# Kernel tuning notes

Hardware: AMD Instinct MI355X
Metric: run time of the kernel (lower is better)

## Reference

```python
import jax, jax.numpy as jnp
import numpy as np

B, S, D, H = 2, 2048, 1024, 16
HD = D // H

def setup_inputs() -> dict:
    key = jax.random.key(0)
    ks = jax.random.split(key, 5)
    s = 1.0 / np.sqrt(D)
    return {
        "x": jax.random.normal(ks[0], (B, S, D), dtype=jnp.float32),
        "Wq": jax.random.normal(ks[1], (D, D), dtype=jnp.float32) * s,
        "Wk": jax.random.normal(ks[2], (D, D), dtype=jnp.float32) * s,
        "Wv": jax.random.normal(ks[3], (D, D), dtype=jnp.float32) * s,
        "Wo": jax.random.normal(ks[4], (D, D), dtype=jnp.float32) * s,
        "bo": jnp.zeros((D,), dtype=jnp.float32),
    }

def reference(x, Wq, Wk, Wv, Wo, bo):
    b, n, _ = x.shape
    # QKV projections (no bias), reshape to [B, H, S, HD]
    def proj(W):
        return (x @ W.T).reshape(b, n, H, HD).transpose(0, 2, 1, 3)
    q, k, v = proj(Wq), proj(Wk), proj(Wv)
    scores = jnp.einsum("bhqd,bhkd->bhqk", q, k)
    causal = jnp.triu(jnp.ones((n, n), dtype=bool), k=1)
    scores = jnp.where(causal, -jnp.inf, scores)
    attn = jax.nn.softmax(scores / np.sqrt(HD), axis=-1)  # dropout p=0.0 (eval)
    ctx = jnp.einsum("bhqk,bhkd->bhqd", attn, v)
    ctx = ctx.transpose(0, 2, 1, 3).reshape(b, n, D)
    return ctx @ Wo.T + bo
```

## Files before the change

### kernel.cpp

```cpp
#include <hip/hip_runtime.h>
#include <stdint.h>


typedef __bf16 bf16_t;
typedef __bf16 bf16x8 __attribute__((ext_vector_type(8)));
typedef float  f32x4  __attribute__((ext_vector_type(4)));
typedef uint32_t u32x4 __attribute__((ext_vector_type(4)));

#define MFMA16(A, B, C) __builtin_amdgcn_mfma_f32_16x16x32_bf16(A, B, C, 0, 0, 0)

__device__ __forceinline__ void async_ld16(const bf16_t* g, bf16_t* l) {
  __builtin_amdgcn_global_load_lds(
      (const __attribute__((address_space(1))) void*)g,
      (__attribute__((address_space(3))) void*)l, 16, 0, 0);
}

__device__ __forceinline__ void cvt4(const float* s, bf16_t* d, int i4) {
  const float4 v = *(const float4*)(s + i4);
  union { uint64_t u; bf16_t h[4]; } pk;
  pk.h[0] = (bf16_t)v.x; pk.h[1] = (bf16_t)v.y;
  pk.h[2] = (bf16_t)v.z; pk.h[3] = (bf16_t)v.w;
  *(uint64_t*)(d + i4) = pk.u;
}

__global__ __launch_bounds__(256) void cvt_all(
    const float* __restrict__ sx, const float* __restrict__ s1,
    const float* __restrict__ s2, const float* __restrict__ s3,
    bf16_t* __restrict__ dx, bf16_t* __restrict__ d1,
    bf16_t* __restrict__ d2, bf16_t* __restrict__ d3) {
  const int y = blockIdx.y;
  if (y != 0 && blockIdx.x >= 1024) return;
  const int i4 = (blockIdx.x * 256 + threadIdx.x) * 4;
  const float* s = (y == 0) ? sx : (y == 1) ? s1 : (y == 2) ? s2 : s3;
  bf16_t*      d = (y == 0) ? dx : (y == 1) ? d1 : (y == 2) ? d2 : d3;
  cvt4(s, d, i4);
}

__global__ __launch_bounds__(256) void cvt_one(const float* __restrict__ s,
                                               bf16_t* __restrict__ d) {
  cvt4(s, d, (blockIdx.x * 256 + threadIdx.x) * 4);
}

__device__ __forceinline__ void gemm_core_async(const bf16_t* __restrict__ A,
                                                const bf16_t* __restrict__ W,
                                                bf16_t* __restrict__ D,
                                                float* __restrict__ Dout,
                                                const float* __restrict__ bias,
                                                int mode) {
  __shared__ __align__(16) bf16_t As[128 * 64];
  __shared__ __align__(16) bf16_t Bs[128 * 64];

  const int tid  = threadIdx.x;
  const int lane = tid & 63;
  const int w    = tid >> 6;
  const int quad = lane >> 4;
  const int l15  = lane & 15;
  const int bm   = blockIdx.y * 128;
  const int bn   = blockIdx.x * 128;
  const int wm   = (w >> 1) * 64;
  const int wn   = (w & 1) * 64;
  const int sr   = lane >> 3;
  const int sc   = lane & 7;

  f32x4 acc[4][4] = {};

  for (int k0 = 0; k0 < 1024; k0 += 64) {
#pragma unroll
    for (int j = 0; j < 4; ++j) {
      const int r0 = w * 32 + j * 8;
      const int r  = r0 + sr;
      const int c  = sc ^ (r & 7);
      async_ld16(A + (size_t)(bm + r) * 1024 + k0 + c * 8, &As[r0 * 64]);
      async_ld16(W + (size_t)(bn + r) * 1024 + k0 + c * 8, &Bs[r0 * 64]);
    }
    __syncthreads();
#pragma unroll
    for (int kk = 0; kk < 64; kk += 32) {
      const int ck = (kk >> 3) + quad;
      bf16x8 aF[4], bF[4];
#pragma unroll
      for (int mt = 0; mt < 4; ++mt) {
        const int r = wm + mt * 16 + l15;
        aF[mt] = *(const bf16x8*)&As[r * 64 + (ck ^ (r & 7)) * 8];
      }
#pragma unroll
      for (int nt = 0; nt < 4; ++nt) {
        const int r = wn + nt * 16 + l15;
        bF[nt] = *(const bf16x8*)&Bs[r * 64 + (ck ^ (r & 7)) * 8];
      }
#pragma unroll
      for (int mt = 0; mt < 4; ++mt)
#pragma unroll
        for (int nt = 0; nt < 4; ++nt)
          acc[mt][nt] = MFMA16(aF[mt], bF[nt], acc[mt][nt]);
    }
    __syncthreads();
  }

#pragma unroll
  for (int mt = 0; mt < 4; ++mt) {
#pragma unroll
    for (int nt = 0; nt < 4; ++nt) {
      const int n  = bn + wn + nt * 16 + l15;
      const int mb = bm + wm + mt * 16 + quad * 4;
      if (mode == 0) {
        const int h = n >> 6, hd = n & 63;
#pragma unroll
        for (int r = 0; r < 4; ++r) {
          const int m = mb + r;
          const int b = m >> 11, s = m & 2047;
          D[(size_t)b * 2097152 + (size_t)h * 131072 + (size_t)s * 64 + hd] =
              (bf16_t)acc[mt][nt][r];
        }
      } else if (mode == 1) {
        const int h = n >> 6, hd = n & 63;
        const int b = mb >> 11, s0 = mb & 2047;
        union { uint64_t u; bf16_t h4[4]; } pk;
#pragma unroll
        for (int r = 0; r < 4; ++r) pk.h4[r] = (bf16_t)acc[mt][nt][r];
        *(uint64_t*)(D + (size_t)b * 2097152 + (size_t)h * 131072 +
                     (size_t)hd * 2048 + s0) = pk.u;
      } else {
        const float bv = bias[n];
#pragma unroll
        for (int r = 0; r < 4; ++r) {
          const int m = mb + r;
          Dout[(size_t)m * 1024 + n] = acc[mt][nt][r] + bv;
        }
      }
    }
  }
}

__global__ __launch_bounds__(256, 2) void gemm_qkv_a(
    const bf16_t* __restrict__ X,  const bf16_t* __restrict__ Wq,
    const bf16_t* __restrict__ Wk, const bf16_t* __restrict__ Wv,
    bf16_t* __restrict__ Q, bf16_t* __restrict__ K, bf16_t* __restrict__ V) {
  const int z = blockIdx.z;
  const bf16_t* W = (z == 0) ? Wq : (z == 1) ? Wk : Wv;
  bf16_t*       D = (z == 0) ? Q  : (z == 1) ? K  : V;
  gemm_core_async(X, W, D, nullptr, nullptr, (z == 2) ? 1 : 0);
}

__global__ __launch_bounds__(256, 2) void gemm_out_a(
    const bf16_t* __restrict__ ctx, const bf16_t* __restrict__ Wo,
    float* __restrict__ out, const float* __restrict__ bo) {
  gemm_core_async(ctx, Wo, nullptr, out, bo, 2);
}

__global__ __launch_bounds__(256, 2) void attn(
    const bf16_t* __restrict__ Qw, const bf16_t* __restrict__ Kw,
    const bf16_t* __restrict__ Vw, bf16_t* __restrict__ ctx) {
  constexpr int LDK = 72, LDV = 136, LDP = 136;
  __shared__ __align__(16) bf16_t Ks[128 * LDK];
  __shared__ __align__(16) bf16_t Vts[64 * LDV];
  __shared__ __align__(16) bf16_t Ps[128 * LDP];

  const int tid  = threadIdx.x;
  const int lane = tid & 63;
  const int w    = tid >> 6;
  const int quad = lane >> 4;
  const int l15  = lane & 15;
  const int b    = blockIdx.z;
  const int h    = blockIdx.y;
  const size_t bh = (size_t)(b * 16 + h) * (size_t)(2048 * 64);
  const bf16_t* Qh = Qw + bh;
  const bf16_t* Kh = Kw + bh;
  const bf16_t* Vh = Vw + bh;

  const int srow = tid >> 3, schk = tid & 7;
  const int vrow = tid >> 4, vchk = tid & 15;

  const float sc_log2 = 0.125f * 1.44269504088896340736f;

  for (int pass = 0; pass < 2; ++pass) {
    const int qt = (pass == 0) ? blockIdx.x : 15 - blockIdx.x;

    __syncthreads();
    bf16_t* Qs = Ps;
    {
      u32x4 rq[4];
#pragma unroll
      for (int s2 = 0; s2 < 4; ++s2)
        rq[s2] = *(const u32x4*)(Qh + (size_t)(qt * 128 + srow + s2 * 32) * 64 + schk * 8);
#pragma unroll
      for (int s2 = 0; s2 < 4; ++s2)
        *(u32x4*)&Qs[(srow + s2 * 32) * LDK + schk * 8] = rq[s2];
    }
    __syncthreads();
    bf16x8 qF[2][2];
#pragma unroll
    for (int kq = 0; kq < 2; ++kq)
#pragma unroll
      for (int k2 = 0; k2 < 2; ++k2)
        qF[kq][k2] = *(const bf16x8*)
            &Qs[(w * 32 + kq * 16 + l15) * LDK + k2 * 32 + quad * 8];

    f32x4 O[2][4] = {};
    float mrow[2] = {-1e30f, -1e30f};
    float lrow[2] = {0.f, 0.f};

    u32x4 rk[4], rv[4];
#pragma unroll
    for (int s2 = 0; s2 < 4; ++s2)
      rk[s2] = *(const u32x4*)(Kh + (size_t)(srow + s2 * 32) * 64 + schk * 8);
#pragma unroll
    for (int s2 = 0; s2 < 4; ++s2)
      rv[s2] = *(const u32x4*)(Vh + (size_t)(vrow + s2 * 16) * 2048 + vchk * 8);

    for (int kt = 0; kt <= qt; ++kt) {
      __syncthreads();
#pragma unroll
      for (int s2 = 0; s2 < 4; ++s2)
        *(u32x4*)&Ks[(srow + s2 * 32) * LDK + schk * 8] = rk[s2];
#pragma unroll
      for (int s2 = 0; s2 < 4; ++s2)
        *(u32x4*)&Vts[(vrow + s2 * 16) * LDV + vchk * 8] = rv[s2];
      __syncthreads();

      if (kt < qt) {
        const int kn = kt + 1;
#pragma unroll
        for (int s2 = 0; s2 < 4; ++s2)
          rk[s2] = *(const u32x4*)(Kh + (size_t)(kn * 128 + srow + s2 * 32) * 64 + schk * 8);
#pragma unroll
        for (int s2 = 0; s2 < 4; ++s2)
          rv[s2] = *(const u32x4*)(Vh + (size_t)(vrow + s2 * 16) * 2048 + kn * 128 + vchk * 8);
      }

      f32x4 St[2][8] = {};
#pragma unroll
      for (int ntk = 0; ntk < 8; ++ntk) {
        const int kr = ntk * 16 + l15;
#pragma unroll
        for (int k2 = 0; k2 < 2; ++k2) {
          const bf16x8 kF = *(const bf16x8*)&Ks[kr * LDK + k2 * 32 + quad * 8];
#pragma unroll
          for (int kq = 0; kq < 2; ++kq)
            St[kq][ntk] = MFMA16(kF, qF[kq][k2], St[kq][ntk]);
        }
      }

      if (kt == qt) {
#pragma unroll
        for (int kq = 0; kq < 2; ++kq) {
          const int ql = w * 32 + kq * 16 + l15;
#pragma unroll
          for (int ntk = 0; ntk < 8; ++ntk)
#pragma unroll
            for (int r = 0; r < 4; ++r)
              if (ntk * 16 + quad * 4 + r > ql) St[kq][ntk][r] = -1e30f;
        }
      }

      float aq[2];
#pragma unroll
      for (int kq = 0; kq < 2; ++kq) {
        float mx = -1e30f;
#pragma unroll
        for (int ntk = 0; ntk < 8; ++ntk)
#pragma unroll
          for (int r = 0; r < 4; ++r) mx = fmaxf(mx, St[kq][ntk][r]);
        mx = fmaxf(mx, __shfl_xor(mx, 16));
        mx = fmaxf(mx, __shfl_xor(mx, 32));
        const float mnew  = fmaxf(mrow[kq], mx);
        const float alpha = exp2f((mrow[kq] - mnew) * sc_log2);
        mrow[kq] = mnew;
        float rs = 0.f;
#pragma unroll
        for (int ntk = 0; ntk < 8; ++ntk) {
          union { uint64_t u; bf16_t h4[4]; } pk;
#pragma unroll
          for (int r = 0; r < 4; ++r) {
            const float p = exp2f((St[kq][ntk][r] - mnew) * sc_log2);
            rs += p;
            pk.h4[r] = (bf16_t)p;
          }
          *(uint64_t*)&Ps[(w * 32 + kq * 16 + l15) * LDP + ntk * 16 + quad * 4] = pk.u;
        }
        rs += __shfl_xor(rs, 16);
        rs += __shfl_xor(rs, 32);
        lrow[kq] = lrow[kq] * alpha + rs;
        aq[kq] = alpha;
      }

#pragma unroll
      for (int mt = 0; mt < 2; ++mt) {
#pragma unroll
        for (int r = 0; r < 4; ++r) {
          const float a = __shfl(aq[mt], quad * 4 + r);
#pragma unroll
          for (int nt = 0; nt < 4; ++nt) O[mt][nt][r] *= a;
        }
      }

#pragma unroll
      for (int kk = 0; kk < 128; kk += 32) {
        const int co = kk + quad * 8;
        bf16x8 pF[2], vF[4];
#pragma unroll
        for (int mt = 0; mt < 2; ++mt)
          pF[mt] = *(const bf16x8*)&Ps[(w * 32 + mt * 16 + l15) * LDP + co];
#pragma unroll
        for (int nt = 0; nt < 4; ++nt)
          vF[nt] = *(const bf16x8*)&Vts[(nt * 16 + l15) * LDV + co];
#pragma unroll
        for (int mt = 0; mt < 2; ++mt)
#pragma unroll
          for (int nt = 0; nt < 4; ++nt)
            O[mt][nt] = MFMA16(pF[mt], vF[nt], O[mt][nt]);
      }
    }

#pragma unroll
    for (int mt = 0; mt < 2; ++mt) {
#pragma unroll
      for (int r = 0; r < 4; ++r) {
        const float lr = __shfl(lrow[mt], quad * 4 + r);
        const float iv = 1.f / lr;
        const int s = qt * 128 + w * 32 + mt * 16 + quad * 4 + r;
#pragma unroll
        for (int nt = 0; nt < 4; ++nt) {
          const int hd = nt * 16 + l15;
          ctx[(size_t)(b * 2048 + s) * 1024 + h * 64 + hd] =
              (bf16_t)(O[mt][nt][r] * iv);
        }
      }
    }
  }
}

extern "C" void kernel_launch(void* const* d_in, const int* in_sizes, int n_in,
                              void* d_out, int out_size, void* d_ws, size_t ws_size,
                              hipStream_t stream) {
  const float* x  = (const float*)d_in[0];
  const float* Wq = (const float*)d_in[1];
  const float* Wk = (const float*)d_in[2];
  const float* Wv = (const float*)d_in[3];
  const float* Wo = (const float*)d_in[4];
  const float* bo = (const float*)d_in[5];

  bf16_t* ws   = (bf16_t*)d_ws;
  bf16_t* Qw   = ws;
  bf16_t* Kw   = ws + 4194304;
  bf16_t* Vw   = ws + 8388608;
  bf16_t* ctxw = ws + 12582912;
  bf16_t* Wob  = Qw;

  bf16_t* dscr = (bf16_t*)d_out;
  bf16_t* xb   = dscr;
  bf16_t* Wqb  = dscr + 4194304;
  bf16_t* Wkb  = dscr + 5242880;
  bf16_t* Wvb  = dscr + 6291456;
  float*  out  = (float*)d_out;

  dim3 blk(256);
  cvt_all<<<dim3(4096, 4), blk, 0, stream>>>(x, Wq, Wk, Wv, xb, Wqb, Wkb, Wvb);
  gemm_qkv_a<<<dim3(8, 32, 3), blk, 0, stream>>>(xb, Wqb, Wkb, Wvb, Qw, Kw, Vw);
  attn<<<dim3(8, 16, 2), blk, 0, stream>>>(Qw, Kw, Vw, ctxw);
  cvt_one<<<dim3(1024), blk, 0, stream>>>(Wo, Wob);
  gemm_out_a<<<dim3(8, 32, 1), blk, 0, stream>>>(ctxw, Wob, out, bo);
}
```

Measured before the change: 194.8 us.

## Split attention passes into separate blocks and fuse Wo conversion into output GEMM

The attention kernel no longer loops over two paired query tiles per block. It launches twice as many blocks, using the batch index to decide whether the query tile is taken forward or mirrored. The output projection becomes a new 64x128-tile GEMM that reads fp32 Wo directly and converts it to bf16 in registers before storing to shared memory. This removes the separate Wo conversion launch and doubles the block count for that GEMM. The trade-offs are lost per-block causal load balancing in attention, and Wo loads that are now synchronous register loads instead of async LDS loads.

```diff
diff --git a/kernel.cpp b/kernel.cpp
--- a/kernel.cpp
+++ b/kernel.cpp
@@ -15,12 +15,15 @@
       (__attribute__((address_space(3))) void*)l, 16, 0, 0);
 }
 
-__device__ __forceinline__ void cvt4(const float* s, bf16_t* d, int i4) {
-  const float4 v = *(const float4*)(s + i4);
-  union { uint64_t u; bf16_t h[4]; } pk;
-  pk.h[0] = (bf16_t)v.x; pk.h[1] = (bf16_t)v.y;
-  pk.h[2] = (bf16_t)v.z; pk.h[3] = (bf16_t)v.w;
-  *(uint64_t*)(d + i4) = pk.u;
+__device__ __forceinline__ u32x4 ld8(const float* p) {
+  const float4 a = *(const float4*)p;
+  const float4 b = *(const float4*)(p + 4);
+  union { u32x4 v; bf16_t h[8]; } r;
+  r.h[0] = (bf16_t)a.x; r.h[1] = (bf16_t)a.y;
+  r.h[2] = (bf16_t)a.z; r.h[3] = (bf16_t)a.w;
+  r.h[4] = (bf16_t)b.x; r.h[5] = (bf16_t)b.y;
+  r.h[6] = (bf16_t)b.z; r.h[7] = (bf16_t)b.w;
+  return r.v;
 }
 
 __global__ __launch_bounds__(256) void cvt_all(
@@ -33,20 +36,22 @@
   const int i4 = (blockIdx.x * 256 + threadIdx.x) * 4;
   const float* s = (y == 0) ? sx : (y == 1) ? s1 : (y == 2) ? s2 : s3;
   bf16_t*      d = (y == 0) ? dx : (y == 1) ? d1 : (y == 2) ? d2 : d3;
-  cvt4(s, d, i4);
-}
-
-__global__ __launch_bounds__(256) void cvt_one(const float* __restrict__ s,
-                                               bf16_t* __restrict__ d) {
-  cvt4(s, d, (blockIdx.x * 256 + threadIdx.x) * 4);
-}
-
-__device__ __forceinline__ void gemm_core_async(const bf16_t* __restrict__ A,
-                                                const bf16_t* __restrict__ W,
-                                                bf16_t* __restrict__ D,
-                                                float* __restrict__ Dout,
-                                                const float* __restrict__ bias,
-                                                int mode) {
+  const float4 v = *(const float4*)(s + i4);
+  union { uint64_t u; bf16_t h[4]; } pk;
+  pk.h[0] = (bf16_t)v.x; pk.h[1] = (bf16_t)v.y;
+  pk.h[2] = (bf16_t)v.z; pk.h[3] = (bf16_t)v.w;
+  *(uint64_t*)(d + i4) = pk.u;
+}
+
+__global__ __launch_bounds__(256, 2) void gemm_qkv_a(
+    const bf16_t* __restrict__ X,  const bf16_t* __restrict__ Wq,
+    const bf16_t* __restrict__ Wk, const bf16_t* __restrict__ Wv,
+    bf16_t* __restrict__ Q, bf16_t* __restrict__ K, bf16_t* __restrict__ V) {
+  const int z = blockIdx.z;
+  const bf16_t* W = (z == 0) ? Wq : (z == 1) ? Wk : Wv;
+  bf16_t*       D = (z == 0) ? Q  : (z == 1) ? K  : V;
+  const int mode = (z == 2) ? 1 : 0;
+
   __shared__ __align__(16) bf16_t As[128 * 64];
   __shared__ __align__(16) bf16_t Bs[128 * 64];
 
@@ -70,7 +75,7 @@
       const int r0 = w * 32 + j * 8;
       const int r  = r0 + sr;
       const int c  = sc ^ (r & 7);
-      async_ld16(A + (size_t)(bm + r) * 1024 + k0 + c * 8, &As[r0 * 64]);
+      async_ld16(X + (size_t)(bm + r) * 1024 + k0 + c * 8, &As[r0 * 64]);
       async_ld16(W + (size_t)(bn + r) * 1024 + k0 + c * 8, &Bs[r0 * 64]);
     }
     __syncthreads();
@@ -103,8 +108,8 @@
     for (int nt = 0; nt < 4; ++nt) {
       const int n  = bn + wn + nt * 16 + l15;
       const int mb = bm + wm + mt * 16 + quad * 4;
+      const int h = n >> 6, hd = n & 63;
       if (mode == 0) {
-        const int h = n >> 6, hd = n & 63;
 #pragma unroll
         for (int r = 0; r < 4; ++r) {
           const int m = mb + r;
@@ -112,40 +117,95 @@
           D[(size_t)b * 2097152 + (size_t)h * 131072 + (size_t)s * 64 + hd] =
               (bf16_t)acc[mt][nt][r];
         }
-      } else if (mode == 1) {
-        const int h = n >> 6, hd = n & 63;
+      } else {
         const int b = mb >> 11, s0 = mb & 2047;
         union { uint64_t u; bf16_t h4[4]; } pk;
 #pragma unroll
         for (int r = 0; r < 4; ++r) pk.h4[r] = (bf16_t)acc[mt][nt][r];
         *(uint64_t*)(D + (size_t)b * 2097152 + (size_t)h * 131072 +
                      (size_t)hd * 2048 + s0) = pk.u;
-      } else {
-        const float bv = bias[n];
-#pragma unroll
-        for (int r = 0; r < 4; ++r) {
-          const int m = mb + r;
-          Dout[(size_t)m * 1024 + n] = acc[mt][nt][r] + bv;
-        }
-      }
-    }
-  }
-}
-
-__global__ __launch_bounds__(256, 2) void gemm_qkv_a(
-    const bf16_t* __restrict__ X,  const bf16_t* __restrict__ Wq,
-    const bf16_t* __restrict__ Wk, const bf16_t* __restrict__ Wv,
-    bf16_t* __restrict__ Q, bf16_t* __restrict__ K, bf16_t* __restrict__ V) {
-  const int z = blockIdx.z;
-  const bf16_t* W = (z == 0) ? Wq : (z == 1) ? Wk : Wv;
-  bf16_t*       D = (z == 0) ? Q  : (z == 1) ? K  : V;
-  gemm_core_async(X, W, D, nullptr, nullptr, (z == 2) ? 1 : 0);
-}
-
-__global__ __launch_bounds__(256, 2) void gemm_out_a(
-    const bf16_t* __restrict__ ctx, const bf16_t* __restrict__ Wo,
+      }
+    }
+  }
+}
+
+__global__ __launch_bounds__(256, 2) void gemm_out_m(
+    const bf16_t* __restrict__ ctx, const float* __restrict__ Wo,
     float* __restrict__ out, const float* __restrict__ bo) {
-  gemm_core_async(ctx, Wo, nullptr, out, bo, 2);
+  __shared__ __align__(16) bf16_t As[64 * 64];
+  __shared__ __align__(16) bf16_t Bs[128 * 64];
+
+  const int tid  = threadIdx.x;
+  const int lane = tid & 63;
+  const int w    = tid >> 6;
+  const int quad = lane >> 4;
+  const int l15  = lane & 15;
+  const int bm   = blockIdx.y * 64;
+  const int bn   = blockIdx.x * 128;
+  const int wm   = (w >> 1) * 32;
+  const int wn   = (w & 1) * 64;
+  const int sr   = lane >> 3;
+  const int sc   = lane & 7;
+  const int srow = tid >> 3;
+  const int schk = tid & 7;
+
+  f32x4 acc[2][4] = {};
+
+  for (int k0 = 0; k0 < 1024; k0 += 64) {
+#pragma unroll
+    for (int j = 0; j < 2; ++j) {
+      const int r0 = w * 16 + j * 8;
+      const int r  = r0 + sr;
+      const int c  = sc ^ (r & 7);
+      async_ld16(ctx + (size_t)(bm + r) * 1024 + k0 + c * 8, &As[r0 * 64]);
+    }
+    u32x4 rb[4];
+#pragma unroll
+    for (int s2 = 0; s2 < 4; ++s2) {
+      const int r = srow + s2 * 32;
+      rb[s2] = ld8(Wo + (size_t)(bn + r) * 1024 + k0 + schk * 8);
+    }
+#pragma unroll
+    for (int s2 = 0; s2 < 4; ++s2) {
+      const int r = srow + s2 * 32;
+      *(u32x4*)&Bs[r * 64 + ((schk ^ (r & 7)) * 8)] = rb[s2];
+    }
+    __syncthreads();
+#pragma unroll
+    for (int kk = 0; kk < 64; kk += 32) {
+      const int ck = (kk >> 3) + quad;
+      bf16x8 aF[2], bF[4];
+#pragma unroll
+      for (int mt = 0; mt < 2; ++mt) {
+        const int r = wm + mt * 16 + l15;
+        aF[mt] = *(const bf16x8*)&As[r * 64 + (ck ^ (r & 7)) * 8];
+      }
+#pragma unroll
+      for (int nt = 0; nt < 4; ++nt) {
+        const int r = wn + nt * 16 + l15;
+        bF[nt] = *(const bf16x8*)&Bs[r * 64 + (ck ^ (r & 7)) * 8];
+      }
+#pragma unroll
+      for (int mt = 0; mt < 2; ++mt)
+#pragma unroll
+        for (int nt = 0; nt < 4; ++nt)
+          acc[mt][nt] = MFMA16(aF[mt], bF[nt], acc[mt][nt]);
+    }
+    __syncthreads();
+  }
+
+#pragma unroll
+  for (int mt = 0; mt < 2; ++mt) {
+#pragma unroll
+    for (int nt = 0; nt < 4; ++nt) {
+      const int n  = bn + wn + nt * 16 + l15;
+      const int mb = bm + wm + mt * 16 + quad * 4;
+      const float bv = bo[n];
+#pragma unroll
+      for (int r = 0; r < 4; ++r)
+        out[(size_t)(mb + r) * 1024 + n] = acc[mt][nt][r] + bv;
+    }
+  }
 }
 
 __global__ __launch_bounds__(256, 2) void attn(
@@ -162,6 +222,7 @@
   const int quad = lane >> 4;
   const int l15  = lane & 15;
   const int b    = blockIdx.z;
+  const int qt   = (b == 0) ? blockIdx.x : 15 - blockIdx.x;
   const int h    = blockIdx.y;
   const size_t bh = (size_t)(b * 16 + h) * (size_t)(2048 * 64);
   const bf16_t* Qh = Qw + bh;
@@ -171,160 +232,155 @@
   const int srow = tid >> 3, schk = tid & 7;
   const int vrow = tid >> 4, vchk = tid & 15;
 
+  bf16_t* Qs = Ps;
+  {
+    u32x4 rq[4];
+#pragma unroll
+    for (int s2 = 0; s2 < 4; ++s2)
+      rq[s2] = *(const u32x4*)(Qh + (size_t)(qt * 128 + srow + s2 * 32) * 64 + schk * 8);
+#pragma unroll
+    for (int s2 = 0; s2 < 4; ++s2)
+      *(u32x4*)&Qs[(srow + s2 * 32) * LDK + schk * 8] = rq[s2];
+  }
+  __syncthreads();
+  bf16x8 qF[2][2];
+#pragma unroll
+  for (int kq = 0; kq < 2; ++kq)
+#pragma unroll
+    for (int k2 = 0; k2 < 2; ++k2)
+      qF[kq][k2] = *(const bf16x8*)
+          &Qs[(w * 32 + kq * 16 + l15) * LDK + k2 * 32 + quad * 8];
+
+  f32x4 O[2][4] = {};
+  float mrow[2] = {-1e30f, -1e30f};
+  float lrow[2] = {0.f, 0.f};
+
   const float sc_log2 = 0.125f * 1.44269504088896340736f;
 
-  for (int pass = 0; pass < 2; ++pass) {
-    const int qt = (pass == 0) ? blockIdx.x : 15 - blockIdx.x;
-
-    __syncthreads();
-    bf16_t* Qs = Ps;
-    {
-      u32x4 rq[4];
+  u32x4 rk[4], rv[4];
+#pragma unroll
+  for (int s2 = 0; s2 < 4; ++s2)
+    rk[s2] = *(const u32x4*)(Kh + (size_t)(srow + s2 * 32) * 64 + schk * 8);
+#pragma unroll
+  for (int s2 = 0; s2 < 4; ++s2)
+    rv[s2] = *(const u32x4*)(Vh + (size_t)(vrow + s2 * 16) * 2048 + vchk * 8);
+
+  for (int kt = 0; kt <= qt; ++kt) {
+    __syncthreads();
+#pragma unroll
+    for (int s2 = 0; s2 < 4; ++s2)
+      *(u32x4*)&Ks[(srow + s2 * 32) * LDK + schk * 8] = rk[s2];
+#pragma unroll
+    for (int s2 = 0; s2 < 4; ++s2)
+      *(u32x4*)&Vts[(vrow + s2 * 16) * LDV + vchk * 8] = rv[s2];
+    __syncthreads();
+
+    if (kt < qt) {
+      const int kn = kt + 1;
 #pragma unroll
       for (int s2 = 0; s2 < 4; ++s2)
-        rq[s2] = *(const u32x4*)(Qh + (size_t)(qt * 128 + srow + s2 * 32) * 64 + schk * 8);
+        rk[s2] = *(const u32x4*)(Kh + (size_t)(kn * 128 + srow + s2 * 32) * 64 + schk * 8);
 #pragma unroll
       for (int s2 = 0; s2 < 4; ++s2)
-        *(u32x4*)&Qs[(srow + s2 * 32) * LDK + schk * 8] = rq[s2];
-    }
-    __syncthreads();
-    bf16x8 qF[2][2];
-#pragma unroll
-    for (int kq = 0; kq < 2; ++kq)
-#pragma unroll
-      for (int k2 = 0; k2 < 2; ++k2)
-        qF[kq][k2] = *(const bf16x8*)
-            &Qs[(w * 32 + kq * 16 + l15) * LDK + k2 * 32 + quad * 8];
-
-    f32x4 O[2][4] = {};
-    float mrow[2] = {-1e30f, -1e30f};
-    float lrow[2] = {0.f, 0.f};
-
-    u32x4 rk[4], rv[4];
-#pragma unroll
-    for (int s2 = 0; s2 < 4; ++s2)
-      rk[s2] = *(const u32x4*)(Kh + (size_t)(srow + s2 * 32) * 64 + schk * 8);
-#pragma unroll
-    for (int s2 = 0; s2 < 4; ++s2)
-      rv[s2] = *(const u32x4*)(Vh + (size_t)(vrow + s2 * 16) * 2048 + vchk * 8);
-
-    for (int kt = 0; kt <= qt; ++kt) {
-      __syncthreads();
-#pragma unroll
-      for (int s2 = 0; s2 < 4; ++s2)
-        *(u32x4*)&Ks[(srow + s2 * 32) * LDK + schk * 8] = rk[s2];
-#pragma unroll
-      for (int s2 = 0; s2 < 4; ++s2)
-        *(u32x4*)&Vts[(vrow + s2 * 16) * LDV + vchk * 8] = rv[s2];
-      __syncthreads();
-
-      if (kt < qt) {
-        const int kn = kt + 1;
-#pragma unroll
-        for (int s2 = 0; s2 < 4; ++s2)
-          rk[s2] = *(const u32x4*)(Kh + (size_t)(kn * 128 + srow + s2 * 32) * 64 + schk * 8);
-#pragma unroll
-        for (int s2 = 0; s2 < 4; ++s2)
-          rv[s2] = *(const u32x4*)(Vh + (size_t)(vrow + s2 * 16) * 2048 + kn * 128 + vchk * 8);
-      }
-
-      f32x4 St[2][8] = {};
+        rv[s2] = *(const u32x4*)(Vh + (size_t)(vrow + s2 * 16) * 2048 + kn * 128 + vchk * 8);
+    }
+
+    f32x4 St[2][8] = {};
+#pragma unroll
+    for (int ntk = 0; ntk < 8; ++ntk) {
+      const int kr = ntk * 16 + l15;
+#pragma unroll
+      for (int k2 = 0; k2 < 2; ++k2) {
+        const bf16x8 kF = *(const bf16x8*)&Ks[kr * LDK + k2 * 32 + quad * 8];
+#pragma unroll
+        for (int kq = 0; kq < 2; ++kq)
+          St[kq][ntk] = MFMA16(kF, qF[kq][k2], St[kq][ntk]);
+      }
+    }
+
+    if (kt == qt) {
+#pragma unroll
+      for (int kq = 0; kq < 2; ++kq) {
+        const int ql = w * 32 + kq * 16 + l15;
+#pragma unroll
+        for (int ntk = 0; ntk < 8; ++ntk)
+#pragma unroll
+          for (int r = 0; r < 4; ++r)
+            if (ntk * 16 + quad * 4 + r > ql) St[kq][ntk][r] = -1e30f;
+      }
+    }
+
+    float aq[2];
+#pragma unroll
+    for (int kq = 0; kq < 2; ++kq) {
+      float mx = -1e30f;
+#pragma unroll
+      for (int ntk = 0; ntk < 8; ++ntk)
+#pragma unroll
+        for (int r = 0; r < 4; ++r) mx = fmaxf(mx, St[kq][ntk][r]);
+      mx = fmaxf(mx, __shfl_xor(mx, 16));
+      mx = fmaxf(mx, __shfl_xor(mx, 32));
+      const float mnew  = fmaxf(mrow[kq], mx);
+      const float alpha = exp2f((mrow[kq] - mnew) * sc_log2);
+      mrow[kq] = mnew;
+      float rs = 0.f;
 #pragma unroll
       for (int ntk = 0; ntk < 8; ++ntk) {
-        const int kr = ntk * 16 + l15;
-#pragma unroll
-        for (int k2 = 0; k2 < 2; ++k2) {
-          const bf16x8 kF = *(const bf16x8*)&Ks[kr * LDK + k2 * 32 + quad * 8];
-#pragma unroll
-          for (int kq = 0; kq < 2; ++kq)
-            St[kq][ntk] = MFMA16(kF, qF[kq][k2], St[kq][ntk]);
+        union { uint64_t u; bf16_t h4[4]; } pk;
+#pragma unroll
+        for (int r = 0; r < 4; ++r) {
+          const float p = exp2f((St[kq][ntk][r] - mnew) * sc_log2);
+          rs += p;
+          pk.h4[r] = (bf16_t)p;
         }
-      }
-
-      if (kt == qt) {
-#pragma unroll
-        for (int kq = 0; kq < 2; ++kq) {
-          const int ql = w * 32 + kq * 16 + l15;
-#pragma unroll
-          for (int ntk = 0; ntk < 8; ++ntk)
-#pragma unroll
-            for (int r = 0; r < 4; ++r)
-              if (ntk * 16 + quad * 4 + r > ql) St[kq][ntk][r] = -1e30f;
-        }
-      }
-
-      float aq[2];
-#pragma unroll
-      for (int kq = 0; kq < 2; ++kq) {
-        float mx = -1e30f;
-#pragma unroll
-        for (int ntk = 0; ntk < 8; ++ntk)
-#pragma unroll
-          for (int r = 0; r < 4; ++r) mx = fmaxf(mx, St[kq][ntk][r]);
-        mx = fmaxf(mx, __shfl_xor(mx, 16));
-        mx = fmaxf(mx, __shfl_xor(mx, 32));
-        const float mnew  = fmaxf(mrow[kq], mx);
-        const float alpha = exp2f((mrow[kq] - mnew) * sc_log2);
-        mrow[kq] = mnew;
-        float rs = 0.f;
-#pragma unroll
-        for (int ntk = 0; ntk < 8; ++ntk) {
-          union { uint64_t u; bf16_t h4[4]; } pk;
-#pragma unroll
-          for (int r = 0; r < 4; ++r) {
-            const float p = exp2f((St[kq][ntk][r] - mnew) * sc_log2);
-            rs += p;
-            pk.h4[r] = (bf16_t)p;
-          }
-          *(uint64_t*)&Ps[(w * 32 + kq * 16 + l15) * LDP + ntk * 16 + quad * 4] = pk.u;
-        }
-        rs += __shfl_xor(rs, 16);
-        rs += __shfl_xor(rs, 32);
-        lrow[kq] = lrow[kq] * alpha + rs;
-        aq[kq] = alpha;
-      }
-
-#pragma unroll
-      for (int mt = 0; mt < 2; ++mt) {
-#pragma unroll
-        for (int r = 0; r < 4; ++r) {
-          const float a = __shfl(aq[mt], quad * 4 + r);
-#pragma unroll
-          for (int nt = 0; nt < 4; ++nt) O[mt][nt][r] *= a;
-        }
-      }
-
-#pragma unroll
-      for (int kk = 0; kk < 128; kk += 32) {
-        const int co = kk + quad * 8;
-        bf16x8 pF[2], vF[4];
-#pragma unroll
-        for (int mt = 0; mt < 2; ++mt)
-          pF[mt] = *(const bf16x8*)&Ps[(w * 32 + mt * 16 + l15) * LDP + co];
+        *(uint64_t*)&Ps[(w * 32 + kq * 16 + l15) * LDP + ntk * 16 + quad * 4] = pk.u;
+      }
+      rs += __shfl_xor(rs, 16);
+      rs += __shfl_xor(rs, 32);
+      lrow[kq] = lrow[kq] * alpha + rs;
+      aq[kq] = alpha;
+    }
+
+#pragma unroll
+    for (int mt = 0; mt < 2; ++mt) {
+#pragma unroll
+      for (int r = 0; r < 4; ++r) {
+        const float a = __shfl(aq[mt], quad * 4 + r);
+#pragma unroll
+        for (int nt = 0; nt < 4; ++nt) O[mt][nt][r] *= a;
+      }
+    }
+
+#pragma unroll
+    for (int kk = 0; kk < 128; kk += 32) {
+      const int co = kk + quad * 8;
+      bf16x8 pF[2], vF[4];
+#pragma unroll
+      for (int mt = 0; mt < 2; ++mt)
+        pF[mt] = *(const bf16x8*)&Ps[(w * 32 + mt * 16 + l15) * LDP + co];
+#pragma unroll
+      for (int nt = 0; nt < 4; ++nt)
+        vF[nt] = *(const bf16x8*)&Vts[(nt * 16 + l15) * LDV + co];
+#pragma unroll
+      for (int mt = 0; mt < 2; ++mt)
 #pragma unroll
         for (int nt = 0; nt < 4; ++nt)
-          vF[nt] = *(const bf16x8*)&Vts[(nt * 16 + l15) * LDV + co];
-#pragma unroll
-        for (int mt = 0; mt < 2; ++mt)
-#pragma unroll
-          for (int nt = 0; nt < 4; ++nt)
-            O[mt][nt] = MFMA16(pF[mt], vF[nt], O[mt][nt]);
-      }
-    }
-
-#pragma unroll
-    for (int mt = 0; mt < 2; ++mt) {
-#pragma unroll
-      for (int r = 0; r < 4; ++r) {
-        const float lr = __shfl(lrow[mt], quad * 4 + r);
-        const float iv = 1.f / lr;
-        const int s = qt * 128 + w * 32 + mt * 16 + quad * 4 + r;
-#pragma unroll
-        for (int nt = 0; nt < 4; ++nt) {
-          const int hd = nt * 16 + l15;
-          ctx[(size_t)(b * 2048 + s) * 1024 + h * 64 + hd] =
-              (bf16_t)(O[mt][nt][r] * iv);
-        }
+          O[mt][nt] = MFMA16(pF[mt], vF[nt], O[mt][nt]);
+    }
+  }
+
+#pragma unroll
+  for (int mt = 0; mt < 2; ++mt) {
+#pragma unroll
+    for (int r = 0; r < 4; ++r) {
+      const float lr = __shfl(lrow[mt], quad * 4 + r);
+      const float iv = 1.f / lr;
+      const int s = qt * 128 + w * 32 + mt * 16 + quad * 4 + r;
+#pragma unroll
+      for (int nt = 0; nt < 4; ++nt) {
+        const int hd = nt * 16 + l15;
+        ctx[(size_t)(b * 2048 + s) * 1024 + h * 64 + hd] =
+            (bf16_t)(O[mt][nt][r] * iv);
       }
     }
   }
@@ -345,7 +401,6 @@
   bf16_t* Kw   = ws + 4194304;
   bf16_t* Vw   = ws + 8388608;
   bf16_t* ctxw = ws + 12582912;
-  bf16_t* Wob  = Qw;
 
   bf16_t* dscr = (bf16_t*)d_out;
   bf16_t* xb   = dscr;
@@ -357,7 +412,6 @@
   dim3 blk(256);
   cvt_all<<<dim3(4096, 4), blk, 0, stream>>>(x, Wq, Wk, Wv, xb, Wqb, Wkb, Wvb);
   gemm_qkv_a<<<dim3(8, 32, 3), blk, 0, stream>>>(xb, Wqb, Wkb, Wvb, Qw, Kw, Vw);
-  attn<<<dim3(8, 16, 2), blk, 0, stream>>>(Qw, Kw, Vw, ctxw);
-  cvt_one<<<dim3(1024), blk, 0, stream>>>(Wo, Wob);
-  gemm_out_a<<<dim3(8, 32, 1), blk, 0, stream>>>(ctxw, Wob, out, bo);
-}
+  attn<<<dim3(16, 16, 2), blk, 0, stream>>>(Qw, Kw, Vw, ctxw);
+  gemm_out_m<<<dim3(8, 64), blk, 0, stream>>>(ctxw, Wo, out, bo);
+}
```

New measurement: 188.5 us. 1.03x faster.
